# Performance work log

Hardware: AMD Instinct MI355X
Metric: run time of the kernel (lower is better)

## Reference

```python
import jax, jax.numpy as jnp
import numpy as np

DIM = 1024
HEADS = 16
DIM_HEAD = 64
INNER = HEADS * DIM_HEAD  # 1024
MLP = 4096
EPS = 1e-5


def layer_norm(x, gamma, beta):
    mu = jnp.mean(x, axis=-1, keepdims=True)
    var = jnp.var(x, axis=-1, keepdims=True)
    return (x - mu) * jax.lax.rsqrt(var + EPS) * gamma + beta


def setup_inputs() -> dict:
    key = jax.random.key(0)
    ks = jax.random.split(key, 10)
    s = 0.02
    return {
        "x": jax.random.normal(ks[0], (2, 2048, DIM), dtype=jnp.float32),
        "ln1_g": jnp.ones((DIM,), jnp.float32),
        "ln1_b": jnp.zeros((DIM,), jnp.float32),
        "w_qkv": jax.random.normal(ks[1], (DIM, 3 * INNER), jnp.float32) * s,
        "w_out": jax.random.normal(ks[2], (INNER, DIM), jnp.float32) * s,
        "b_out": jnp.zeros((DIM,), jnp.float32),
        "ln2_g": jnp.ones((DIM,), jnp.float32),
        "ln2_b": jnp.zeros((DIM,), jnp.float32),
        "w1": jax.random.normal(ks[3], (DIM, MLP), jnp.float32) * s,
        "b1": jnp.zeros((MLP,), jnp.float32),
        "w2": jax.random.normal(ks[4], (MLP, DIM), jnp.float32) * s,
        "b2": jnp.zeros((DIM,), jnp.float32),
    }


def reference(x, ln1_g, ln1_b, w_qkv, w_out, b_out, ln2_g, ln2_b, w1, b1, w2, b2):
    b, n, _ = x.shape
    scale = DIM_HEAD ** -0.5

    # --- attention sublayer (pre-norm) ---
    h = layer_norm(x, ln1_g, ln1_b)
    qkv = h @ w_qkv  # [b, n, 3*inner]
    q, k, v = jnp.split(qkv, 3, axis=-1)
    # [b, n, inner] -> [b, heads, n, dim_head]
    def to_heads(t):
        return t.reshape(b, n, HEADS, DIM_HEAD).transpose(0, 2, 1, 3)
    q, k, v = to_heads(q), to_heads(k), to_heads(v)
    dots = jnp.einsum('bhid,bhjd->bhij', q, k) * scale  # [b,h,n,n]
    attn = jax.nn.softmax(dots, axis=-1)
    out = jnp.einsum('bhij,bhjd->bhid', attn, v)
    out = out.transpose(0, 2, 1, 3).reshape(b, n, INNER)
    x = out @ w_out + b_out + x

    # --- FFN sublayer (pre-norm) ---
    h = layer_norm(x, ln2_g, ln2_b)
    h = jax.nn.gelu(h @ w1 + b1, approximate=False)
    x = h @ w2 + b2 + x
    return x
```

## Files before the change

kernel.cpp:

```cpp
#include <hip/hip_runtime.h>
#include <hip/hip_bf16.h>
#include <math.h>

#define SEQ 2048
#define BATCH 2
#define TOKENS 4096
#define HEADS 16
#define DHEAD 64
#define TOKSTRIDE 3072

typedef __attribute__((ext_vector_type(4))) float f32x4;
typedef __attribute__((ext_vector_type(16))) float f32x16;
typedef __attribute__((ext_vector_type(8))) __bf16 bf16x8;
typedef __attribute__((ext_vector_type(8))) unsigned short ushort8;
typedef __attribute__((ext_vector_type(4))) unsigned short ushort4_t;
typedef __attribute__((ext_vector_type(4))) unsigned u32x4;

#if __has_builtin(__builtin_amdgcn_exp2f)
#define EXP2(x) __builtin_amdgcn_exp2f(x)
#else
#define EXP2(x) exp2f(x)
#endif

__device__ __forceinline__ unsigned short f2bf(float f) {
  unsigned u = __builtin_bit_cast(unsigned, f);
  u += 0x7fffu + ((u >> 16) & 1u);
  return (unsigned short)(u >> 16);
}

__device__ __forceinline__ float bf2f(unsigned short s) {
  unsigned u = ((unsigned)s) << 16;
  return __builtin_bit_cast(float, u);
}

__device__ __forceinline__ unsigned cvt_pk_bf16(float lo, float hi) {
  unsigned r;
  asm("v_cvt_pk_bf16_f32 %0, %1, %2" : "=v"(r) : "v"(lo), "v"(hi));
  return r;
}

__device__ __forceinline__ void cp16(const void* g, void* l) {
  __builtin_amdgcn_global_load_lds((const __attribute__((address_space(1))) void*)g,
                                   (__attribute__((address_space(3))) void*)l, 16, 0, 0);
}

__global__ __launch_bounds__(256) void ln_rows(const float* __restrict__ x,
                                               const float* __restrict__ g,
                                               const float* __restrict__ b,
                                               unsigned short* __restrict__ out) {
  const int row = blockIdx.x;
  const int t = threadIdx.x;
  const f32x4* x4 = (const f32x4*)(x + (size_t)row * 1024);
  f32x4 v = x4[t];
  float sum = v[0] + v[1] + v[2] + v[3];
  float ss  = v[0]*v[0] + v[1]*v[1] + v[2]*v[2] + v[3]*v[3];
#pragma unroll
  for (int off = 1; off < 64; off <<= 1) {
    sum += __shfl_xor(sum, off);
    ss  += __shfl_xor(ss, off);
  }
  __shared__ float red[8];
  const int w = t >> 6, l = t & 63;
  if (l == 0) { red[w] = sum; red[w + 4] = ss; }
  __syncthreads();
  sum = red[0] + red[1] + red[2] + red[3];
  ss  = red[4] + red[5] + red[6] + red[7];
  const float mean = sum * (1.0f / 1024.0f);
  const float var  = ss * (1.0f / 1024.0f) - mean * mean;
  const float rs = rsqrtf(var + 1e-5f);
  ushort4_t o;
#pragma unroll
  for (int j = 0; j < 4; ++j) {
    float gv = g[t * 4 + j], bv = b[t * 4 + j];
    o[j] = f2bf((v[j] - mean) * rs * gv + bv);
  }
  *(ushort4_t*)(out + (size_t)row * 1024 + t * 4) = o;
}

__global__ __launch_bounds__(256) void transpose_cast(const float* __restrict__ w,
                                                      unsigned short* __restrict__ wt,
                                                      int K, int N, float scale, int nscaled) {
  __shared__ float tile[32][33];
  const int n0 = blockIdx.x * 32, k0 = blockIdx.y * 32;
  const int tx = threadIdx.x & 31;
  const int ty = threadIdx.x >> 5;
#pragma unroll
  for (int i = 0; i < 4; ++i)
    tile[ty + 8 * i][tx] = w[(size_t)(k0 + ty + 8 * i) * N + n0 + tx];
  __syncthreads();
#pragma unroll
  for (int i = 0; i < 4; ++i) {
    int n = n0 + ty + 8 * i;
    float s = (n < nscaled) ? scale : 1.0f;
    wt[(size_t)n * K + k0 + tx] = f2bf(tile[tx][ty + 8 * i] * s);
  }
}

template <int EPI, int BN>
__global__ __launch_bounds__(256, 2) void gemm_bt(
    const unsigned short* __restrict__ A, const unsigned short* __restrict__ Bt,
    void* __restrict__ Cp, const float* __restrict__ bias, const float* __restrict__ res,
    int M, int N, int K) {
  constexpr int BM = 128, BK = 64;
  constexpr int MR = BM / 32, NR = BN / 32;
  constexpr int AIT = BM * BK / 2048;
  constexpr int BIT = BN * BK / 2048;
  __shared__ unsigned short la[BM * BK];
  __shared__ unsigned short lb[BN * BK];
  const int t = threadIdx.x;
  const int w = t >> 6, l = t & 63;
  const int nwg = gridDim.x;
  const int bid = blockIdx.x;
  const int bid2 = (bid & 7) * (nwg >> 3) + (bid >> 3);
  const int nx = N / BN;
  const int m0 = (bid2 / nx) * BM, n0 = (bid2 % nx) * BN;
  const int wr = w >> 1, wc = w & 1;
  const int lrow = l & 15, lk4 = l >> 4;
  f32x4 acc[MR][NR] = {};

  for (int k0 = 0; k0 < K; k0 += BK) {
#pragma unroll
    for (int i = 0; i < AIT; ++i) {
      int idx = t + 256 * i;
      int row = idx >> 3, seg = idx & 7;
      int ss = seg ^ (row & 7);
      cp16(A + (size_t)(m0 + row) * K + k0 + ss * 8, (char*)la + w * 1024 + i * 4096);
    }
#pragma unroll
    for (int i = 0; i < BIT; ++i) {
      int idx = t + 256 * i;
      int row = idx >> 3, seg = idx & 7;
      int ss = seg ^ (row & 7);
      cp16(Bt + (size_t)(n0 + row) * K + k0 + ss * 8, (char*)lb + w * 1024 + i * 4096);
    }
    __syncthreads();
#pragma unroll
    for (int ks = 0; ks < 2; ++ks) {
      bf16x8 af[MR], bfr[NR];
#pragma unroll
      for (int mi = 0; mi < MR; ++mi) {
        int row = wr * (BM / 2) + mi * 16 + lrow;
        int ss = (ks * 4 + lk4) ^ (row & 7);
        af[mi] = *(const bf16x8*)((const char*)la + row * 128 + ss * 16);
      }
#pragma unroll
      for (int ni = 0; ni < NR; ++ni) {
        int row = wc * (BN / 2) + ni * 16 + lrow;
        int ss = (ks * 4 + lk4) ^ (row & 7);
        bfr[ni] = *(const bf16x8*)((const char*)lb + row * 128 + ss * 16);
      }
#pragma unroll
      for (int mi = 0; mi < MR; ++mi)
#pragma unroll
        for (int ni = 0; ni < NR; ++ni)
          acc[mi][ni] = __builtin_amdgcn_mfma_f32_16x16x32_bf16(af[mi], bfr[ni], acc[mi][ni], 0, 0, 0);
    }
    __syncthreads();
  }

#pragma unroll
  for (int mi = 0; mi < MR; ++mi) {
    int rowb = m0 + wr * (BM / 2) + mi * 16 + lk4 * 4;
#pragma unroll
    for (int ni = 0; ni < NR; ++ni) {
      int col = n0 + wc * (BN / 2) + ni * 16 + lrow;
      f32x4 a = acc[mi][ni];
#pragma unroll
      for (int r = 0; r < 4; ++r) {
        size_t off = (size_t)(rowb + r) * N + col;
        if (EPI == 0) {
          ((unsigned short*)Cp)[off] = f2bf(a[r]);
        } else if (EPI == 1) {
          ((float*)Cp)[off] = a[r] + bias[col] + res[off];
        } else {
          float v = a[r] + bias[col];
          ((unsigned short*)Cp)[off] = f2bf(0.5f * v * (1.0f + erff(v * 0.70710678f)));
        }
      }
    }
  }
}

__global__ __launch_bounds__(256, 2) void attn2(const unsigned short* __restrict__ qkv,
                                                unsigned short* __restrict__ Op,
                                                float2* __restrict__ ml) {
  __shared__ unsigned short lk_[2][64 * 64];
  __shared__ unsigned short lvt[2][64 * 64];
  const int t = threadIdx.x, wv = t >> 6, l = t & 63;
  const int chunk = blockIdx.x & 1, qb = blockIdx.x >> 1;
  const int h = blockIdx.y, b = blockIdx.z;
  const size_t tok0 = (size_t)b * SEQ;
  const int lq = l & 31, hi = l >> 5, l7 = l & 7;
  const int qrow = qb * 128 + wv * 32 + lq;
  const int kstart = chunk * 16;

  bf16x8 qf[4];
#pragma unroll
  for (int dc = 0; dc < 4; ++dc)
    qf[dc] = *(const bf16x8*)(qkv + (tok0 + qrow) * TOKSTRIDE + h * DHEAD + dc * 16 + hi * 8);

  float mrun = -1e30f, lsum = 0.0f;
  f32x16 o0 = {}, o1 = {};

  {
#pragma unroll
    for (int i = 0; i < 2; ++i) {
      int idx = t + 256 * i;
      int key = idx >> 3, seg = idx & 7;
      cp16(qkv + (tok0 + kstart * 64 + key) * TOKSTRIDE + 1024 + h * DHEAD + ((seg ^ (key & 7)) << 3),
           (char*)lk_[0] + wv * 1024 + i * 4096);
    }
#pragma unroll
    for (int i = 0; i < 2; ++i) {
      int idx = t + 256 * i;
      int key = idx & 63, seg = idx >> 6;
      ushort8 v8 = *(const ushort8*)(qkv + (tok0 + kstart * 64 + key) * TOKSTRIDE + 2048 + h * DHEAD + seg * 8);
#pragma unroll
      for (int j = 0; j < 8; ++j) {
        int d = seg * 8 + j;
        lvt[0][d * 64 + (((key >> 3) ^ (d & 7)) << 3) + (key & 7)] = v8[j];
      }
    }
  }
  __syncthreads();

  int cur = 0;
  for (int kb = 0; kb < 16; ++kb) {
    const int nxt = cur ^ 1;
    const int kpre = kstart + ((kb + 1 < 16) ? kb + 1 : kb);
#pragma unroll
    for (int i = 0; i < 2; ++i) {
      int idx = t + 256 * i;
      int key = idx >> 3, seg = idx & 7;
      cp16(qkv + (tok0 + kpre * 64 + key) * TOKSTRIDE + 1024 + h * DHEAD + ((seg ^ (key & 7)) << 3),
           (char*)lk_[nxt] + wv * 1024 + i * 4096);
    }
    ushort8 vpre[2];
#pragma unroll
    for (int i = 0; i < 2; ++i) {
      int idx = t + 256 * i;
      int key = idx & 63, seg = idx >> 6;
      vpre[i] = *(const ushort8*)(qkv + (tok0 + kpre * 64 + key) * TOKSTRIDE + 2048 + h * DHEAD + seg * 8);
    }

    f32x16 s0 = {}, s1 = {};
    __builtin_amdgcn_s_setprio(1);
#pragma unroll
    for (int dc = 0; dc < 4; ++dc) {
      int sgA = (dc * 2 + hi) ^ l7;
      bf16x8 kf0 = *(const bf16x8*)((const char*)lk_[cur] + lq * 128 + (sgA << 4));
      bf16x8 kf1 = *(const bf16x8*)((const char*)lk_[cur] + (32 + lq) * 128 + (sgA << 4));
      s0 = __builtin_amdgcn_mfma_f32_32x32x16_bf16(kf0, qf[dc], s0, 0, 0, 0);
      s1 = __builtin_amdgcn_mfma_f32_32x32x16_bf16(kf1, qf[dc], s1, 0, 0, 0);
    }
    __builtin_amdgcn_s_setprio(0);

    float mx[16];
#pragma unroll
    for (int r = 0; r < 16; ++r) mx[r] = fmaxf(s0[r], s1[r]);
#pragma unroll
    for (int st = 8; st > 0; st >>= 1)
#pragma unroll
      for (int r = 0; r < 8; ++r)
        if (r < st) mx[r] = fmaxf(mx[r], mx[r + st]);
    float pm = fmaxf(mx[0], __shfl_xor(mx[0], 32));

    if (__any(pm > mrun + 8.0f)) {
      float mn = fmaxf(mrun, pm);
      float alpha = EXP2(mrun - mn);
      mrun = mn;
      lsum *= alpha;
#pragma unroll
      for (int r = 0; r < 16; ++r) {
        int qi = (r & 3) + 8 * (r >> 2) + 4 * hi;
        float ar = __shfl(alpha, qi);
        o0[r] *= ar; o1[r] *= ar;
      }
    }

    float p0[16], p1[16];
    float psA = 0.f, psB = 0.f;
#pragma unroll
    for (int r = 0; r < 16; ++r) { p0[r] = EXP2(s0[r] - mrun); psA += p0[r]; }
#pragma unroll
    for (int r = 0; r < 16; ++r) { p1[r] = EXP2(s1[r] - mrun); psB += p1[r]; }
    float psum = psA + psB;
    psum += __shfl_xor(psum, 32);
    lsum += psum;

    unsigned W0[8], W1[8], X0[8], X1[8];
#pragma unroll
    for (int mI = 0; mI < 8; ++mI) {
      W0[mI] = cvt_pk_bf16(p0[2 * mI], p0[2 * mI + 1]);
      W1[mI] = cvt_pk_bf16(p1[2 * mI], p1[2 * mI + 1]);
    }
#pragma unroll
    for (int mI = 0; mI < 8; ++mI) {
      X0[mI] = __shfl_xor((int)W0[mI], 32);
      X1[mI] = __shfl_xor((int)W1[mI], 32);
    }

    __builtin_amdgcn_s_setprio(1);
#pragma unroll
    for (int kt = 0; kt < 2; ++kt) {
#pragma unroll
      for (int c = 0; c < 2; ++c) {
        u32x4 fw;
        if (kt == 0) {
          fw[0] = hi ? X0[4 * c + 2] : W0[4 * c + 0];
          fw[1] = hi ? X0[4 * c + 3] : W0[4 * c + 1];
          fw[2] = hi ? W0[4 * c + 2] : X0[4 * c + 0];
          fw[3] = hi ? W0[4 * c + 3] : X0[4 * c + 1];
        } else {
          fw[0] = hi ? X1[4 * c + 2] : W1[4 * c + 0];
          fw[1] = hi ? X1[4 * c + 3] : W1[4 * c + 1];
          fw[2] = hi ? W1[4 * c + 2] : X1[4 * c + 0];
          fw[3] = hi ? W1[4 * c + 3] : X1[4 * c + 1];
        }
        bf16x8 pf = __builtin_bit_cast(bf16x8, fw);
        int ksg = (kt * 4 + c * 2 + hi) ^ l7;
        bf16x8 vfA = *(const bf16x8*)((const char*)lvt[cur] + lq * 128 + (ksg << 4));
        bf16x8 vfB = *(const bf16x8*)((const char*)lvt[cur] + (32 + lq) * 128 + (ksg << 4));
        o0 = __builtin_amdgcn_mfma_f32_32x32x16_bf16(pf, vfA, o0, 0, 0, 0);
        o1 = __builtin_amdgcn_mfma_f32_32x32x16_bf16(pf, vfB, o1, 0, 0, 0);
      }
    }
    __builtin_amdgcn_s_setprio(0);

#pragma unroll
    for (int i = 0; i < 2; ++i) {
      int idx = t + 256 * i;
      int key = idx & 63, seg = idx >> 6;
#pragma unroll
      for (int j = 0; j < 8; ++j) {
        int d = seg * 8 + j;
        lvt[nxt][d * 64 + (((key >> 3) ^ (d & 7)) << 3) + (key & 7)] = vpre[i][j];
      }
    }
    __syncthreads();
    cur = nxt;
  }

  const size_t cbase = (size_t)chunk * TOKENS;
#pragma unroll
  for (int r = 0; r < 16; ++r) {
    int qi = (r & 3) + 8 * (r >> 2) + 4 * hi;
    size_t rowoff = (cbase + tok0 + qb * 128 + wv * 32 + qi) * (size_t)1024 + h * DHEAD;
    Op[rowoff + lq]      = f2bf(o0[r]);
    Op[rowoff + 32 + lq] = f2bf(o1[r]);
  }
  if (l < 32) {
    size_t tokr = tok0 + qb * 128 + wv * 32 + lq;
    ml[(cbase + tokr) * 16 + h] = make_float2(mrun, lsum);
  }
}

__global__ __launch_bounds__(256) void attn_combine(const unsigned short* __restrict__ Op,
                                                    const float2* __restrict__ ml,
                                                    unsigned short* __restrict__ out) {
  const int t = threadIdx.x, w = t >> 6, l = t & 63;
  const size_t tok = blockIdx.x * 4 + w;
#pragma unroll
  for (int h = 0; h < 16; ++h) {
    float2 a = ml[tok * 16 + h];
    float2 c = ml[((size_t)TOKENS + tok) * 16 + h];
    float M = fmaxf(a.x, c.x);
    float w0 = EXP2(a.x - M), w1 = EXP2(c.x - M);
    float inv = 1.0f / (a.y * w0 + c.y * w1);
    int col = h * 64 + l;
    float o = (bf2f(Op[tok * 1024 + col]) * w0 +
               bf2f(Op[((size_t)TOKENS + tok) * 1024 + col]) * w1) * inv;
    out[tok * 1024 + col] = f2bf(o);
  }
}

extern "C" void kernel_launch(void* const* d_in, const int* in_sizes, int n_in,
                              void* d_out, int out_size, void* d_ws, size_t ws_size,
                              hipStream_t stream) {
  const float* x    = (const float*)d_in[0];
  const float* ln1g = (const float*)d_in[1];
  const float* ln1b = (const float*)d_in[2];
  const float* wqkv = (const float*)d_in[3];
  const float* wout = (const float*)d_in[4];
  const float* bout = (const float*)d_in[5];
  const float* ln2g = (const float*)d_in[6];
  const float* ln2b = (const float*)d_in[7];
  const float* w1   = (const float*)d_in[8];
  const float* b1   = (const float*)d_in[9];
  const float* w2   = (const float*)d_in[10];
  const float* b2   = (const float*)d_in[11];

  char* ws = (char*)d_ws;
  unsigned short* wqkvT = (unsigned short*)ws; ws += (size_t)3072 * 1024 * 2;
  unsigned short* woutT = (unsigned short*)ws; ws += (size_t)1024 * 1024 * 2;
  unsigned short* w1T   = (unsigned short*)ws; ws += (size_t)4096 * 1024 * 2;
  unsigned short* w2T   = (unsigned short*)ws; ws += (size_t)1024 * 4096 * 2;
  unsigned short* h1    = (unsigned short*)ws; ws += (size_t)TOKENS * 1024 * 2;
  unsigned short* qkvb  = (unsigned short*)ws; ws += (size_t)TOKENS * 3072 * 2;
  unsigned short* attno = (unsigned short*)ws; ws += (size_t)TOKENS * 1024 * 2;
  float*          xa    = (float*)ws;          ws += (size_t)TOKENS * 1024 * 4;
  unsigned short* h2    = (unsigned short*)ws; ws += (size_t)TOKENS * 1024 * 2;
  unsigned short* hid   = (unsigned short*)ws; ws += (size_t)TOKENS * 4096 * 2;
  float2*         mlbuf = (float2*)ws;         ws += (size_t)2 * TOKENS * 16 * 8;
  unsigned short* Opart = hid;

  transpose_cast<<<dim3(3072 / 32, 1024 / 32), 256, 0, stream>>>(wqkv, wqkvT, 1024, 3072, 0.18033688f, 1024);
  transpose_cast<<<dim3(1024 / 32, 1024 / 32), 256, 0, stream>>>(wout, woutT, 1024, 1024, 1.0f, 0);
  transpose_cast<<<dim3(4096 / 32, 1024 / 32), 256, 0, stream>>>(w1, w1T, 1024, 4096, 1.0f, 0);
  transpose_cast<<<dim3(1024 / 32, 4096 / 32), 256, 0, stream>>>(w2, w2T, 4096, 1024, 1.0f, 0);

  ln_rows<<<TOKENS, 256, 0, stream>>>(x, ln1g, ln1b, h1);
  gemm_bt<0, 128><<<768, 256, 0, stream>>>(h1, wqkvT, qkvb, nullptr, nullptr, TOKENS, 3072, 1024);
  attn2<<<dim3(2 * SEQ / 128, HEADS, BATCH), 256, 0, stream>>>(qkvb, Opart, mlbuf);
  attn_combine<<<TOKENS / 4, 256, 0, stream>>>(Opart, mlbuf, attno);
  gemm_bt<1, 64><<<512, 256, 0, stream>>>(attno, woutT, xa, bout, x, TOKENS, 1024, 1024);
  ln_rows<<<TOKENS, 256, 0, stream>>>(xa, ln2g, ln2b, h2);
  gemm_bt<2, 128><<<1024, 256, 0, stream>>>(h2, w1T, hid, b1, nullptr, TOKENS, 4096, 1024);
  gemm_bt<1, 64><<<512, 256, 0, stream>>>(hid, w2T, (float*)d_out, b2, xa, TOKENS, 1024, 4096);
}
```

Baseline: 261.2 us.

## Add 256x256-tile 512-thread GEMM for QKV and FFN1 projections

```diff
diff --git a/kernel.cpp b/kernel.cpp
--- a/kernel.cpp
+++ b/kernel.cpp
@@ -181,6 +181,99 @@
   }
 }
 
+template <int EPI>
+__global__ __launch_bounds__(512, 2) void gemm256(
+    const unsigned short* __restrict__ A, const unsigned short* __restrict__ Bt,
+    void* __restrict__ Cp, const float* __restrict__ bias,
+    int M, int N, int K) {
+  __shared__ unsigned short lds[65536];
+  const int t = threadIdx.x;
+  const int w = t >> 6, l = t & 63;
+  const int nwg = gridDim.x;
+  const int bid = blockIdx.x;
+  const int bid2 = (bid & 7) * (nwg >> 3) + (bid >> 3);
+  const int nx = N / 256;
+  const int m0 = (bid2 / nx) * 256, n0 = (bid2 % nx) * 256;
+  const int wr = w >> 2, wc = w & 3;
+  const int lrow = l & 15, lk4 = l >> 4;
+  f32x4 acc[8][4] = {};
+
+  const int NT = K >> 5;
+
+#define STAGE256(kt)                                                              \
+  {                                                                               \
+    char* dst = (char*)lds + ((kt) & 3) * 65536 / 2;                              \
+    _Pragma("unroll") for (int i = 0; i < 2; ++i) {                               \
+      int idx = t + 512 * i;                                                      \
+      int row = idx >> 2, seg = idx & 3;                                          \
+      int ss = seg ^ (row & 3);                                                   \
+      cp16(A + (size_t)(m0 + row) * K + (kt) * 32 + ss * 8, dst + t * 16 + i * 8192); \
+      cp16(Bt + (size_t)(n0 + row) * K + (kt) * 32 + ss * 8, dst + 16384 + t * 16 + i * 8192); \
+    }                                                                             \
+  }
+
+#define COMPUTE256(kt)                                                            \
+  {                                                                               \
+    const char* ab = (const char*)lds + ((kt) & 3) * 32768;                       \
+    const char* bb = ab + 16384;                                                  \
+    bf16x8 af[8], bfr[4];                                                         \
+    _Pragma("unroll") for (int mi = 0; mi < 8; ++mi) {                            \
+      int row = wr * 128 + mi * 16 + lrow;                                        \
+      af[mi] = *(const bf16x8*)(ab + row * 64 + ((lk4 ^ (row & 3)) << 4));        \
+    }                                                                             \
+    _Pragma("unroll") for (int ni = 0; ni < 4; ++ni) {                            \
+      int row = wc * 64 + ni * 16 + lrow;                                         \
+      bfr[ni] = *(const bf16x8*)(bb + row * 64 + ((lk4 ^ (row & 3)) << 4));       \
+    }                                                                             \
+    __builtin_amdgcn_s_setprio(1);                                                \
+    _Pragma("unroll") for (int mi = 0; mi < 8; ++mi)                              \
+      _Pragma("unroll") for (int ni = 0; ni < 4; ++ni)                            \
+        acc[mi][ni] = __builtin_amdgcn_mfma_f32_16x16x32_bf16(af[mi], bfr[ni], acc[mi][ni], 0, 0, 0); \
+    __builtin_amdgcn_s_setprio(0);                                                \
+  }
+
+  STAGE256(0);
+  STAGE256(1);
+
+  for (int kt = 0; kt < NT - 2; ++kt) {
+    STAGE256(kt + 2);
+    asm volatile("s_waitcnt vmcnt(8)" ::: "memory");
+    __builtin_amdgcn_s_barrier();
+    __builtin_amdgcn_sched_barrier(0);
+    COMPUTE256(kt);
+  }
+  asm volatile("s_waitcnt vmcnt(4)" ::: "memory");
+  __builtin_amdgcn_s_barrier();
+  __builtin_amdgcn_sched_barrier(0);
+  COMPUTE256(NT - 2);
+  asm volatile("s_waitcnt vmcnt(0)" ::: "memory");
+  __builtin_amdgcn_s_barrier();
+  __builtin_amdgcn_sched_barrier(0);
+  COMPUTE256(NT - 1);
+#undef STAGE256
+#undef COMPUTE256
+
+#pragma unroll
+  for (int mi = 0; mi < 8; ++mi) {
+    int rowb = m0 + wr * 128 + mi * 16 + lk4 * 4;
+#pragma unroll
+    for (int ni = 0; ni < 4; ++ni) {
+      int col = n0 + wc * 64 + ni * 16 + lrow;
+      f32x4 a = acc[mi][ni];
+#pragma unroll
+      for (int r = 0; r < 4; ++r) {
+        size_t off = (size_t)(rowb + r) * N + col;
+        if (EPI == 0) {
+          ((unsigned short*)Cp)[off] = f2bf(a[r]);
+        } else {
+          float v = a[r] + bias[col];
+          ((unsigned short*)Cp)[off] = f2bf(0.5f * v * (1.0f + erff(v * 0.70710678f)));
+        }
+      }
+    }
+  }
+}
+
 __global__ __launch_bounds__(256, 2) void attn2(const unsigned short* __restrict__ qkv,
                                                 unsigned short* __restrict__ Op,
                                                 float2* __restrict__ ml) {
@@ -410,11 +503,11 @@
   transpose_cast<<<dim3(1024 / 32, 4096 / 32), 256, 0, stream>>>(w2, w2T, 4096, 1024, 1.0f, 0);
 
   ln_rows<<<TOKENS, 256, 0, stream>>>(x, ln1g, ln1b, h1);
-  gemm_bt<0, 128><<<768, 256, 0, stream>>>(h1, wqkvT, qkvb, nullptr, nullptr, TOKENS, 3072, 1024);
+  gemm256<0><<<192, 512, 0, stream>>>(h1, wqkvT, qkvb, nullptr, TOKENS, 3072, 1024);
   attn2<<<dim3(2 * SEQ / 128, HEADS, BATCH), 256, 0, stream>>>(qkvb, Opart, mlbuf);
   attn_combine<<<TOKENS / 4, 256, 0, stream>>>(Opart, mlbuf, attno);
   gemm_bt<1, 64><<<512, 256, 0, stream>>>(attno, woutT, xa, bout, x, TOKENS, 1024, 1024);
   ln_rows<<<TOKENS, 256, 0, stream>>>(xa, ln2g, ln2b, h2);
-  gemm_bt<2, 128><<<1024, 256, 0, stream>>>(h2, w1T, hid, b1, nullptr, TOKENS, 4096, 1024);
+  gemm256<2><<<256, 512, 0, stream>>>(h2, w1T, hid, b1, TOKENS, 4096, 1024);
   gemm_bt<1, 64><<<512, 256, 0, stream>>>(hid, w2T, (float*)d_out, b2, xa, TOKENS, 1024, 4096);
 }
```

New measurement: 264.6 us. About the same (+1.3%).

## Replace GEMM with 4-stage LDS pipelined 32x32 MFMA kernel and larger FFN tiles

Applied to the files above, without the earlier changes.

```diff
diff --git a/kernel.cpp b/kernel.cpp
--- a/kernel.cpp
+++ b/kernel.cpp
@@ -96,78 +96,99 @@
   }
 }
 
-template <int EPI, int BN>
-__global__ __launch_bounds__(256, 2) void gemm_bt(
+template <int EPI, int BM, int BN, int WM, int WN>
+__global__ __launch_bounds__(WM * WN * 64) void gemmP(
     const unsigned short* __restrict__ A, const unsigned short* __restrict__ Bt,
     void* __restrict__ Cp, const float* __restrict__ bias, const float* __restrict__ res,
     int M, int N, int K) {
-  constexpr int BM = 128, BK = 64;
-  constexpr int MR = BM / 32, NR = BN / 32;
-  constexpr int AIT = BM * BK / 2048;
-  constexpr int BIT = BN * BK / 2048;
-  __shared__ unsigned short la[BM * BK];
-  __shared__ unsigned short lb[BN * BK];
+  constexpr int THREADS = WM * WN * 64;
+  constexpr int MR = BM / (WM * 32);
+  constexpr int NR = BN / (WN * 32);
+  constexpr int AIT = (BM * 64) / (THREADS * 16);
+  constexpr int BIT = (BN * 64) / (THREADS * 16);
+  constexpr int TILEB = (BM + BN) * 64;
+  __shared__ char lds[4 * TILEB];
   const int t = threadIdx.x;
   const int w = t >> 6, l = t & 63;
+  const int lq = l & 31, hi = l >> 5;
+  const int wr = w / WN, wc = w % WN;
   const int nwg = gridDim.x;
   const int bid = blockIdx.x;
   const int bid2 = (bid & 7) * (nwg >> 3) + (bid >> 3);
   const int nx = N / BN;
   const int m0 = (bid2 / nx) * BM, n0 = (bid2 % nx) * BN;
-  const int wr = w >> 1, wc = w & 1;
-  const int lrow = l & 15, lk4 = l >> 4;
-  f32x4 acc[MR][NR] = {};
-
-  for (int k0 = 0; k0 < K; k0 += BK) {
-#pragma unroll
-    for (int i = 0; i < AIT; ++i) {
-      int idx = t + 256 * i;
-      int row = idx >> 3, seg = idx & 7;
-      int ss = seg ^ (row & 7);
-      cp16(A + (size_t)(m0 + row) * K + k0 + ss * 8, (char*)la + w * 1024 + i * 4096);
-    }
-#pragma unroll
-    for (int i = 0; i < BIT; ++i) {
-      int idx = t + 256 * i;
-      int row = idx >> 3, seg = idx & 7;
-      int ss = seg ^ (row & 7);
-      cp16(Bt + (size_t)(n0 + row) * K + k0 + ss * 8, (char*)lb + w * 1024 + i * 4096);
-    }
-    __syncthreads();
-#pragma unroll
-    for (int ks = 0; ks < 2; ++ks) {
-      bf16x8 af[MR], bfr[NR];
-#pragma unroll
-      for (int mi = 0; mi < MR; ++mi) {
-        int row = wr * (BM / 2) + mi * 16 + lrow;
-        int ss = (ks * 4 + lk4) ^ (row & 7);
-        af[mi] = *(const bf16x8*)((const char*)la + row * 128 + ss * 16);
-      }
-#pragma unroll
-      for (int ni = 0; ni < NR; ++ni) {
-        int row = wc * (BN / 2) + ni * 16 + lrow;
-        int ss = (ks * 4 + lk4) ^ (row & 7);
-        bfr[ni] = *(const bf16x8*)((const char*)lb + row * 128 + ss * 16);
-      }
-#pragma unroll
-      for (int mi = 0; mi < MR; ++mi)
-#pragma unroll
-        for (int ni = 0; ni < NR; ++ni)
-          acc[mi][ni] = __builtin_amdgcn_mfma_f32_16x16x32_bf16(af[mi], bfr[ni], acc[mi][ni], 0, 0, 0);
-    }
-    __syncthreads();
-  }
+  f32x16 acc[MR][NR] = {};
+  const int NT = K >> 5;
+
+#define STAGEP(kt)                                                                   \
+  {                                                                                  \
+    char* dst = lds + ((kt) & 3) * TILEB;                                            \
+    _Pragma("unroll") for (int i = 0; i < AIT; ++i) {                                \
+      int idx = t + THREADS * i;                                                     \
+      int row = idx >> 2, seg = idx & 3;                                             \
+      cp16(A + (size_t)(m0 + row) * K + (kt) * 32 + ((seg ^ (row & 3)) << 3),        \
+           dst + idx * 16);                                                          \
+    }                                                                                \
+    _Pragma("unroll") for (int i = 0; i < BIT; ++i) {                                \
+      int idx = t + THREADS * i;                                                     \
+      int row = idx >> 2, seg = idx & 3;                                             \
+      cp16(Bt + (size_t)(n0 + row) * K + (kt) * 32 + ((seg ^ (row & 3)) << 3),       \
+           dst + BM * 64 + idx * 16);                                                \
+    }                                                                                \
+  }
+
+#define COMPUTEP(kt)                                                                 \
+  {                                                                                  \
+    const char* ab = lds + ((kt) & 3) * TILEB;                                       \
+    const char* bb = ab + BM * 64;                                                   \
+    _Pragma("unroll") for (int ks = 0; ks < 2; ++ks) {                               \
+      bf16x8 af[MR], bf[NR];                                                         \
+      _Pragma("unroll") for (int mi = 0; mi < MR; ++mi) {                            \
+        int row = wr * (MR * 32) + mi * 32 + lq;                                     \
+        af[mi] = *(const bf16x8*)(ab + row * 64 + (((ks * 2 + hi) ^ (row & 3)) << 4)); \
+      }                                                                              \
+      _Pragma("unroll") for (int ni = 0; ni < NR; ++ni) {                            \
+        int row = wc * (NR * 32) + ni * 32 + lq;                                     \
+        bf[ni] = *(const bf16x8*)(bb + row * 64 + (((ks * 2 + hi) ^ (row & 3)) << 4)); \
+      }                                                                              \
+      __builtin_amdgcn_s_setprio(1);                                                 \
+      _Pragma("unroll") for (int mi = 0; mi < MR; ++mi)                              \
+        _Pragma("unroll") for (int ni = 0; ni < NR; ++ni)                            \
+          acc[mi][ni] = __builtin_amdgcn_mfma_f32_32x32x16_bf16(af[mi], bf[ni], acc[mi][ni], 0, 0, 0); \
+      __builtin_amdgcn_s_setprio(0);                                                 \
+    }                                                                                \
+  }
+
+  STAGEP(0);
+  STAGEP(1);
+  for (int kt = 0; kt < NT - 2; ++kt) {
+    STAGEP(kt + 2);
+    asm volatile("s_waitcnt vmcnt(%0)" ::"i"(2 * (AIT + BIT)) : "memory");
+    __builtin_amdgcn_s_barrier();
+    __builtin_amdgcn_sched_barrier(0);
+    COMPUTEP(kt);
+  }
+  asm volatile("s_waitcnt vmcnt(%0)" ::"i"(AIT + BIT) : "memory");
+  __builtin_amdgcn_s_barrier();
+  __builtin_amdgcn_sched_barrier(0);
+  COMPUTEP(NT - 2);
+  asm volatile("s_waitcnt vmcnt(0)" ::: "memory");
+  __builtin_amdgcn_s_barrier();
+  __builtin_amdgcn_sched_barrier(0);
+  COMPUTEP(NT - 1);
+#undef STAGEP
+#undef COMPUTEP
 
 #pragma unroll
   for (int mi = 0; mi < MR; ++mi) {
-    int rowb = m0 + wr * (BM / 2) + mi * 16 + lk4 * 4;
 #pragma unroll
     for (int ni = 0; ni < NR; ++ni) {
-      int col = n0 + wc * (BN / 2) + ni * 16 + lrow;
-      f32x4 a = acc[mi][ni];
-#pragma unroll
-      for (int r = 0; r < 4; ++r) {
-        size_t off = (size_t)(rowb + r) * N + col;
+      f32x16 a = acc[mi][ni];
+      int col = n0 + wc * (NR * 32) + ni * 32 + lq;
+#pragma unroll
+      for (int r = 0; r < 16; ++r) {
+        int row = m0 + wr * (MR * 32) + mi * 32 + (r & 3) + 8 * (r >> 2) + 4 * hi;
+        size_t off = (size_t)row * N + col;
         if (EPI == 0) {
           ((unsigned short*)Cp)[off] = f2bf(a[r]);
         } else if (EPI == 1) {
@@ -410,11 +431,11 @@
   transpose_cast<<<dim3(1024 / 32, 4096 / 32), 256, 0, stream>>>(w2, w2T, 4096, 1024, 1.0f, 0);
 
   ln_rows<<<TOKENS, 256, 0, stream>>>(x, ln1g, ln1b, h1);
-  gemm_bt<0, 128><<<768, 256, 0, stream>>>(h1, wqkvT, qkvb, nullptr, nullptr, TOKENS, 3072, 1024);
+  gemmP<0, 128, 128, 2, 2><<<768, 256, 0, stream>>>(h1, wqkvT, qkvb, nullptr, nullptr, TOKENS, 3072, 1024);
   attn2<<<dim3(2 * SEQ / 128, HEADS, BATCH), 256, 0, stream>>>(qkvb, Opart, mlbuf);
   attn_combine<<<TOKENS / 4, 256, 0, stream>>>(Opart, mlbuf, attno);
-  gemm_bt<1, 64><<<512, 256, 0, stream>>>(attno, woutT, xa, bout, x, TOKENS, 1024, 1024);
+  gemmP<1, 128, 64, 2, 2><<<512, 256, 0, stream>>>(attno, woutT, xa, bout, x, TOKENS, 1024, 1024);
   ln_rows<<<TOKENS, 256, 0, stream>>>(xa, ln2g, ln2b, h2);
-  gemm_bt<2, 128><<<1024, 256, 0, stream>>>(h2, w1T, hid, b1, nullptr, TOKENS, 4096, 1024);
-  gemm_bt<1, 64><<<512, 256, 0, stream>>>(hid, w2T, (float*)d_out, b2, xa, TOKENS, 1024, 4096);
-}
+  gemmP<2, 256, 256, 2, 4><<<256, 512, 0, stream>>>(h2, w1T, hid, b1, nullptr, TOKENS, 4096, 1024);
+  gemmP<1, 128, 64, 2, 2><<<512, 256, 0, stream>>>(hid, w2T, (float*)d_out, b2, xa, TOKENS, 1024, 4096);
+}
```

Result: slower. 282.8 us, median of 2 (+8.3%).
